# Performance work log

Measured on AMD Instinct MI355X. Metric: run time of the kernel, lower is better.

The kernel has to match this reference:

```python
import jax, jax.numpy as jnp
import numpy as np

B, T, H, W, C = 2, 4, 128, 128, 192
HEADS = 6
WS = 8          # attention window (per-frame, wsD=1)
OW = 12         # overlapping KV window: 8 + int(8*0.5)
PAD = (OW - WS) // 2
TBL = (WS + OW - 1) ** 2   # 361 relative-position-bias entries
MLP_HID = C * 2


def setup_inputs() -> dict:
    key = jax.random.key(0)
    ks = jax.random.split(key, 8)
    s = 0.02
    return dict(
        x=jax.random.normal(ks[0], (B, T, H, W, C), jnp.float32),
        x_size=jnp.array([H, W], jnp.int32),  # unused by forward (shadowed), kept for signature fidelity
        rpi_oca=jax.random.randint(ks[1], (WS * WS, OW * OW), 0, TBL),
        norm1_g=jnp.ones((C,), jnp.float32), norm1_b=jnp.zeros((C,), jnp.float32),
        qkv_w=jax.random.normal(ks[2], (C, 3 * C), jnp.float32) * s,
        qkv_b=jnp.zeros((3 * C,), jnp.float32),
        rpb_table=jax.random.normal(ks[3], (TBL, HEADS), jnp.float32) * s,
        norm2_g=jnp.ones((C,), jnp.float32), norm2_b=jnp.zeros((C,), jnp.float32),
        fc1_w=jax.random.normal(ks[4], (C, MLP_HID), jnp.float32) * s,
        fc1_b=jnp.zeros((MLP_HID,), jnp.float32),
        fc2_w=jax.random.normal(ks[5], (MLP_HID, C), jnp.float32) * s,
        fc2_b=jnp.zeros((C,), jnp.float32),
    )


def _ln(x, g, b):
    m = x.mean(-1, keepdims=True)
    v = ((x - m) ** 2).mean(-1, keepdims=True)
    return (x - m) * jax.lax.rsqrt(v + 1e-5) * g + b


def reference(x, x_size, rpi_oca, norm1_g, norm1_b, qkv_w, qkv_b, rpb_table,
              norm2_g, norm2_b, fc1_w, fc1_b, fc2_w, fc2_b):
    b, t, h, w, c = x.shape
    d = c // HEADS
    scale = d ** -0.5
    nH, nW = h // WS, w // WS
    b_ = b * t * nH * nW  # total windows
    shortcut = x
    xn = _ln(x, norm1_g, norm1_b)
    qkv = (xn @ qkv_w + qkv_b).reshape(b, t, h, w, 3, c)
    q, k, v = qkv[..., 0, :], qkv[..., 1, :], qkv[..., 2, :]
    # --- query: non-overlapping (1,8,8) windows -> (b_, heads, 64, d)
    qw = (q.reshape(b, t, nH, WS, nW, WS, c)
           .transpose(0, 1, 2, 4, 3, 5, 6)
           .reshape(b_, WS * WS, HEADS, d)
           .transpose(0, 2, 1, 3))
    # --- key/value: overlapping (1,12,12) windows with stride 8, zero-padded by 2
    hid = (jnp.arange(nH) * WS)[:, None] + jnp.arange(OW)  # (nH, OW)
    wid = (jnp.arange(nW) * WS)[:, None] + jnp.arange(OW)  # (nW, OW)

    def owin(z):
        zp = jnp.pad(z, ((0, 0), (0, 0), (PAD, PAD), (PAD, PAD), (0, 0)))
        zw = zp[:, :, hid][:, :, :, :, wid]  # (b, t, nH, OW, nW, OW, c)
        return (zw.transpose(0, 1, 2, 4, 3, 5, 6)
                  .reshape(b_, OW * OW, HEADS, d)
                  .transpose(0, 2, 1, 3))

    kw, vw = owin(k), owin(v)
    attn = jnp.einsum('bhqd,bhkd->bhqk', qw * scale, kw)  # (b_, heads, 64, 144)
    bias = rpb_table[rpi_oca.reshape(-1)].reshape(WS * WS, OW * OW, HEADS).transpose(2, 0, 1)
    attn = attn + bias[None]  # NOTE: original forward applies NO softmax (self.softmax unused)
    out = (jnp.einsum('bhqk,bhkd->bhqd', attn, vw)
             .transpose(0, 2, 1, 3)
             .reshape(b_, WS * WS, c))
    # window_reverse
    xa = (out.reshape(b, t, nH, nW, WS, WS, c)
             .transpose(0, 1, 2, 4, 3, 5, 6)
             .reshape(b, t, h, w, c))
    x = xa + shortcut  # self.proj is never applied in the original forward
    hmlp = jax.nn.gelu(_ln(x, norm2_g, norm2_b) @ fc1_w + fc1_b, approximate=False)
    return x + (hmlp @ fc2_w + fc2_b)
```

## Files before the change

kernel.cpp:

```cpp
#include <hip/hip_runtime.h>
#include <cstdint>
#include <cstddef>

typedef short bf16x8 __attribute__((ext_vector_type(8)));
typedef unsigned short u16x4 __attribute__((ext_vector_type(4)));
typedef float f32x4  __attribute__((ext_vector_type(4)));
typedef unsigned short u16;

#define DEVI __device__ __forceinline__

constexpr int C     = 192;
constexpr int HEADS = 6;
constexpr int NQKV  = 576;
constexpr int HID   = 384;
constexpr int NTOK  = 131072;

DEVI u16 f2bf(float f){
  union { float f; unsigned u; } v; v.f = f;
  return (u16)((v.u + 0x7fffu + ((v.u >> 16) & 1u)) >> 16);
}

DEVI float gelu(float xx){
  float y  = xx * 0.70710678118654752f;
  float ay = fabsf(y);
  float t  = __builtin_amdgcn_rcpf(1.0f + 0.3275911f * ay);
  float p  = t*(0.254829592f + t*(-0.284496736f + t*(1.421413741f + t*(-1.453152027f + t*1.061405429f))));
  float e  = __expf(-(y*y));
  float er = copysignf(1.0f - p*e, y);
  return 0.5f * xx * (1.0f + er);
}

__global__ void prep_kernel(const float* __restrict__ qkv_w,
                            const float* __restrict__ fc1_w,
                            const float* __restrict__ fc2_w,
                            const int*   __restrict__ rpi,
                            const float* __restrict__ rpb,
                            u16* __restrict__ qkvP,
                            u16* __restrict__ fc1P,
                            u16* __restrict__ fc2P,
                            float* __restrict__ bias_pk){
  int idx = blockIdx.x * blockDim.x + threadIdx.x;
  int stride = gridDim.x * blockDim.x;
  for(int i = idx; i < 36*6*64*8; i += stride){
    int e = i & 7, lane = (i >> 3) & 63, t = i >> 9;
    int ks = t % 6, p = t / 6;
    int n = p*16 + (lane & 15), k = ks*32 + (lane >> 4)*8 + e;
    qkvP[i] = f2bf(qkv_w[k*NQKV + n]);
  }
  for(int i = idx; i < 24*6*64*8; i += stride){
    int e = i & 7, lane = (i >> 3) & 63, t = i >> 9;
    int ks = t % 6, p = t / 6;
    int n = p*16 + (lane & 15), k = ks*32 + (lane >> 4)*8 + e;
    fc1P[i] = f2bf(fc1_w[k*HID + n]);
  }
  for(int i = idx; i < 12*12*64*8; i += stride){
    int e = i & 7, lane = (i >> 3) & 63, t = i >> 9;
    int ks = t % 12, p = t / 12;
    int n = p*16 + (lane & 15), k = ks*32 + (lane >> 4)*8 + e;
    fc2P[i] = f2bf(fc2_w[k*C + n]);
  }
  const int n4 = HEADS*5*2*4*64*4;
  for(int i = idx; i < n4; i += stride){
    int t = i;
    int r    = t & 3;  t >>= 2;
    int lane = t & 63; t >>= 6;
    int mi   = t & 3;  t >>= 2;
    int nf   = t & 1;  t >>= 1;
    int chunk = t % 5; int head = t / 5;
    int g = lane >> 4, col = lane & 15;
    int q  = mi*16 + g*4 + r;
    int kk = chunk*32 + nf*16 + col;
    float v = 0.f;
    if(kk < 144) v = rpb[rpi[q*144 + kk]*HEADS + head];
    bias_pk[i] = v;
  }
}

__global__ __launch_bounds__(384, 4)
void qkv_kernel(const float* __restrict__ x,
                const float* __restrict__ g1,
                const float* __restrict__ b1,
                const u16* __restrict__ wP,
                const float* __restrict__ qb,
                u16* __restrict__ qkv){
  __shared__ u16 xn[64][200];
  __shared__ u16 rp[64][152];
  const int tid = threadIdx.x;
  const int bid = blockIdx.x;
  const int nh = (bid >> 3) & 1;
  const int tb = (bid & 7) + ((bid >> 4) << 3);
  const size_t tok0 = (size_t)tb * 64;
  if(tid < 256){
    const int trow = tid >> 2;
    const int j = tid & 3;
    const float* xr = x + (tok0 + trow)*C;
    float4 xv[12];
    #pragma unroll
    for(int u = 0; u < 12; ++u)
      xv[u] = *reinterpret_cast<const float4*>(xr + u*16 + j*4);
    float s1 = 0.f, s2 = 0.f;
    #pragma unroll
    for(int u = 0; u < 12; ++u){
      const float* f = reinterpret_cast<const float*>(&xv[u]);
      #pragma unroll
      for(int e = 0; e < 4; ++e){ s1 += f[e]; s2 += f[e]*f[e]; }
    }
    s1 += __shfl_xor(s1, 1, 64); s2 += __shfl_xor(s2, 1, 64);
    s1 += __shfl_xor(s1, 2, 64); s2 += __shfl_xor(s2, 2, 64);
    const float mean = s1 * (1.f/192.f);
    const float rstd = rsqrtf(s2*(1.f/192.f) - mean*mean + 1e-5f);
    #pragma unroll
    for(int u = 0; u < 12; ++u){
      const float4 gv = *reinterpret_cast<const float4*>(g1 + u*16 + j*4);
      const float4 bv = *reinterpret_cast<const float4*>(b1 + u*16 + j*4);
      const float* f = reinterpret_cast<const float*>(&xv[u]);
      const float* gp = reinterpret_cast<const float*>(&gv);
      const float* bp = reinterpret_cast<const float*>(&bv);
      u16x4 pk;
      #pragma unroll
      for(int e = 0; e < 4; ++e) pk[e] = f2bf((f[e] - mean)*rstd*gp[e] + bp[e]);
      *reinterpret_cast<u16x4*>(&xn[trow][u*16 + j*4]) = pk;
    }
  }
  __syncthreads();
  const int lane = tid & 63;
  const int wn = tid >> 6;
  const int g = lane >> 4, col = lane & 15;
  const f32x4 fzero = {0.f, 0.f, 0.f, 0.f};
  f32x4 acc[4][3];
  #pragma unroll
  for(int mi = 0; mi < 4; ++mi)
    #pragma unroll
    for(int nf = 0; nf < 3; ++nf) acc[mi][nf] = fzero;
  const int p0 = nh*18 + wn*3;
  #pragma unroll
  for(int ks = 0; ks < 6; ++ks){
    bf16x8 wf[3];
    #pragma unroll
    for(int nf = 0; nf < 3; ++nf)
      wf[nf] = *reinterpret_cast<const bf16x8*>(wP + ((size_t)(((p0 + nf)*6 + ks)*64) + lane)*8);
    bf16x8 a[4];
    #pragma unroll
    for(int mi = 0; mi < 4; ++mi)
      a[mi] = *reinterpret_cast<const bf16x8*>(&xn[mi*16 + col][ks*32 + g*8]);
    #pragma unroll
    for(int nf = 0; nf < 3; ++nf)
      #pragma unroll
      for(int mi = 0; mi < 4; ++mi)
        acc[mi][nf] = __builtin_amdgcn_mfma_f32_16x16x32_bf16(a[mi], wf[nf], acc[mi][nf], 0, 0, 0);
  }
  #pragma unroll
  for(int ph = 0; ph < 2; ++ph){
    if((wn >> 1) + (wn >> 2) == ph*2 ? false : true){}
    if(wn >= ph*3 && wn < ph*3 + 3){
      const int wl = wn - ph*3;
      #pragma unroll
      for(int mi = 0; mi < 4; ++mi){
        #pragma unroll
        for(int nf = 0; nf < 3; ++nf){
          const int nloc = wl*48 + nf*16 + col;
          const float bb = qb[nh*288 + ph*144 + nloc];
          #pragma unroll
          for(int r = 0; r < 4; ++r)
            rp[mi*16 + g*4 + r][nloc] = f2bf(acc[mi][nf][r] + bb);
        }
      }
    }
    __syncthreads();
    #pragma unroll
    for(int it = 0; it < 3; ++it){
      const int c = tid + it*384;
      const int tok = c / 18, cc = c - tok*18;
      const int n0 = nh*288 + ph*144 + cc*8;
      const int pl = n0 >> 5, d0 = n0 & 31;
      bf16x8 vv = *reinterpret_cast<const bf16x8*>(&rp[tok][cc*8]);
      *reinterpret_cast<bf16x8*>(qkv + ((size_t)pl*NTOK + tok0 + tok)*32 + d0) = vv;
    }
    __syncthreads();
  }
}

__global__ __launch_bounds__(64, 2)
void attn_kernel(const u16* __restrict__ qkv,
                 const float* __restrict__ bias_pk,
                 const float* __restrict__ x,
                 float* __restrict__ out){
  __shared__ u16 Vt[32][168];
  __shared__ u16 Pl[64][40];
  const int lane = threadIdx.x;
  const int g = lane >> 4, col = lane & 15;
  const int win = blockIdx.x, head = blockIdx.y;
  const int bt = win >> 8, wh = (win >> 4) & 15, ww = win & 15;
  const int h0 = wh*8, w0 = ww*8;
  const size_t tokbase = (size_t)bt * 16384;
  const u16* Qp = qkv + (size_t)head      *NTOK*32;
  const u16* Kp = qkv + (size_t)(6 + head)*NTOK*32;
  const u16* Vp = qkv + (size_t)(12 + head)*NTOK*32;
  bf16x8 kf[10];
  #pragma unroll
  for(int i = 0; i < 10; ++i){
    const int kr = i*16 + col;
    const int r12 = (kr*2731) >> 15;
    const int c12 = kr - r12*12;
    const int hh = h0 - 2 + r12;
    const int wp = w0 - 2 + c12;
    bf16x8 kv_ = {0,0,0,0,0,0,0,0};
    bf16x8 vv_ = {0,0,0,0,0,0,0,0};
    if(kr < 144 && hh >= 0 && hh < 128 && wp >= 0 && wp < 128){
      const size_t t = tokbase + hh*128 + wp;
      kv_ = *reinterpret_cast<const bf16x8*>(Kp + t*32 + g*8);
      vv_ = *reinterpret_cast<const bf16x8*>(Vp + t*32 + g*8);
    }
    kf[i] = kv_;
    #pragma unroll
    for(int e = 0; e < 8; ++e) Vt[g*8 + e][kr] = (u16)vv_[e];
  }
  bf16x8 qf[4];
  #pragma unroll
  for(int mi = 0; mi < 4; ++mi){
    const int row = mi*16 + col;
    const size_t t = tokbase + (size_t)(h0 + (row >> 3))*128 + w0 + (row & 7);
    qf[mi] = *reinterpret_cast<const bf16x8*>(Qp + t*32 + g*8);
  }
  const f32x4 fzero = {0.f, 0.f, 0.f, 0.f};
  f32x4 oacc[4][2];
  #pragma unroll
  for(int mi = 0; mi < 4; ++mi){ oacc[mi][0] = fzero; oacc[mi][1] = fzero; }
  const float scale = 0.17677669529663689f;
  for(int ch = 0; ch < 5; ++ch){
    f32x4 s[4][2];
    #pragma unroll
    for(int nf = 0; nf < 2; ++nf){
      const bf16x8 kk = kf[ch*2 + nf];
      #pragma unroll
      for(int mi = 0; mi < 4; ++mi)
        s[mi][nf] = __builtin_amdgcn_mfma_f32_16x16x32_bf16(qf[mi], kk, fzero, 0, 0, 0);
    }
    #pragma unroll
    for(int nf = 0; nf < 2; ++nf){
      #pragma unroll
      for(int mi = 0; mi < 4; ++mi){
        const float4 bv = *reinterpret_cast<const float4*>(
            bias_pk + (size_t)((((head*5 + ch)*2 + nf)*4 + mi)*64 + lane)*4);
        const float* bvp = reinterpret_cast<const float*>(&bv);
        #pragma unroll
        for(int r = 0; r < 4; ++r)
          Pl[mi*16 + g*4 + r][nf*16 + col] = f2bf(s[mi][nf][r]*scale + bvp[r]);
      }
    }
    bf16x8 pa[4];
    #pragma unroll
    for(int mi = 0; mi < 4; ++mi)
      pa[mi] = *reinterpret_cast<const bf16x8*>(&Pl[mi*16 + col][g*8]);
    #pragma unroll
    for(int nf = 0; nf < 2; ++nf){
      const bf16x8 vfr = *reinterpret_cast<const bf16x8*>(&Vt[nf*16 + col][ch*32 + g*8]);
      #pragma unroll
      for(int mi = 0; mi < 4; ++mi)
        oacc[mi][nf] = __builtin_amdgcn_mfma_f32_16x16x32_bf16(pa[mi], vfr, oacc[mi][nf], 0, 0, 0);
    }
  }
  #pragma unroll
  for(int mi = 0; mi < 4; ++mi){
    #pragma unroll
    for(int nf = 0; nf < 2; ++nf){
      #pragma unroll
      for(int r = 0; r < 4; ++r){
        const int row = mi*16 + g*4 + r;
        const int hh = h0 + (row >> 3), wp = w0 + (row & 7);
        const size_t o = (tokbase + hh*128 + wp)*(size_t)C + head*32 + nf*16 + col;
        out[o] = oacc[mi][nf][r] + x[o];
      }
    }
  }
}

__global__ __launch_bounds__(512, 4)
void mlp_kernel(float* __restrict__ io,
                const float* __restrict__ g2,
                const float* __restrict__ b2,
                const u16* __restrict__ w1P,
                const float* __restrict__ fb1,
                const u16* __restrict__ w2P,
                const float* __restrict__ fb2){
  __shared__ u16 xn[64][200];
  __shared__ u16 hl[64][200];
  const int tid = threadIdx.x;
  const size_t tok0 = (size_t)blockIdx.x * 64;
  {
    const int trow = tid >> 3;
    const int j = tid & 7;
    const float* xr = io + (tok0 + trow)*C;
    float4 xv[6];
    #pragma unroll
    for(int u = 0; u < 6; ++u)
      xv[u] = *reinterpret_cast<const float4*>(xr + u*32 + j*4);
    float s1 = 0.f, s2 = 0.f;
    #pragma unroll
    for(int u = 0; u < 6; ++u){
      const float* f = reinterpret_cast<const float*>(&xv[u]);
      #pragma unroll
      for(int e = 0; e < 4; ++e){ s1 += f[e]; s2 += f[e]*f[e]; }
    }
    s1 += __shfl_xor(s1, 1, 64); s2 += __shfl_xor(s2, 1, 64);
    s1 += __shfl_xor(s1, 2, 64); s2 += __shfl_xor(s2, 2, 64);
    s1 += __shfl_xor(s1, 4, 64); s2 += __shfl_xor(s2, 4, 64);
    const float mean = s1 * (1.f/192.f);
    const float rstd = rsqrtf(s2*(1.f/192.f) - mean*mean + 1e-5f);
    #pragma unroll
    for(int u = 0; u < 6; ++u){
      const float4 gv = *reinterpret_cast<const float4*>(g2 + u*32 + j*4);
      const float4 bv = *reinterpret_cast<const float4*>(b2 + u*32 + j*4);
      const float* f = reinterpret_cast<const float*>(&xv[u]);
      const float* gp = reinterpret_cast<const float*>(&gv);
      const float* bp = reinterpret_cast<const float*>(&bv);
      u16x4 pk;
      #pragma unroll
      for(int e = 0; e < 4; ++e) pk[e] = f2bf((f[e] - mean)*rstd*gp[e] + bp[e]);
      *reinterpret_cast<u16x4*>(&xn[trow][u*32 + j*4]) = pk;
    }
  }
  __syncthreads();
  const int lane = tid & 63, wave = tid >> 6;
  const int wm = wave >> 2;
  const int wn = wave & 3;
  const int g = lane >> 4, col = lane & 15;
  const f32x4 fzero = {0.f, 0.f, 0.f, 0.f};
  f32x4 acc2[2][3];
  #pragma unroll
  for(int mi = 0; mi < 2; ++mi)
    #pragma unroll
    for(int nf = 0; nf < 3; ++nf) acc2[mi][nf] = fzero;
  #pragma unroll
  for(int hb = 0; hb < 2; ++hb){
    f32x4 acc1[2][3];
    #pragma unroll
    for(int mi = 0; mi < 2; ++mi)
      #pragma unroll
      for(int nf = 0; nf < 3; ++nf) acc1[mi][nf] = fzero;
    #pragma unroll
    for(int ks = 0; ks < 6; ++ks){
      bf16x8 wf[3];
      #pragma unroll
      for(int nf = 0; nf < 3; ++nf)
        wf[nf] = *reinterpret_cast<const bf16x8*>(w1P + ((size_t)(((hb*12 + wn*3 + nf)*6 + ks)*64) + lane)*8);
      bf16x8 a[2];
      #pragma unroll
      for(int mi = 0; mi < 2; ++mi)
        a[mi] = *reinterpret_cast<const bf16x8*>(&xn[wm*32 + mi*16 + col][ks*32 + g*8]);
      #pragma unroll
      for(int nf = 0; nf < 3; ++nf)
        #pragma unroll
        for(int mi = 0; mi < 2; ++mi)
          acc1[mi][nf] = __builtin_amdgcn_mfma_f32_16x16x32_bf16(a[mi], wf[nf], acc1[mi][nf], 0, 0, 0);
    }
    #pragma unroll
    for(int mi = 0; mi < 2; ++mi){
      #pragma unroll
      for(int nf = 0; nf < 3; ++nf){
        const int nl = wn*48 + nf*16 + col;
        const float bb = fb1[hb*192 + nl];
        #pragma unroll
        for(int r = 0; r < 4; ++r){
          const int row = wm*32 + mi*16 + g*4 + r;
          hl[row][nl] = f2bf(gelu(acc1[mi][nf][r] + bb));
        }
      }
    }
    __syncthreads();
    #pragma unroll
    for(int ks = 0; ks < 6; ++ks){
      bf16x8 wf[3];
      #pragma unroll
      for(int nf = 0; nf < 3; ++nf)
        wf[nf] = *reinterpret_cast<const bf16x8*>(w2P + ((size_t)(((wn*3 + nf)*12 + hb*6 + ks)*64) + lane)*8);
      bf16x8 a[2];
      #pragma unroll
      for(int mi = 0; mi < 2; ++mi)
        a[mi] = *reinterpret_cast<const bf16x8*>(&hl[wm*32 + mi*16 + col][ks*32 + g*8]);
      #pragma unroll
      for(int nf = 0; nf < 3; ++nf)
        #pragma unroll
        for(int mi = 0; mi < 2; ++mi)
          acc2[mi][nf] = __builtin_amdgcn_mfma_f32_16x16x32_bf16(a[mi], wf[nf], acc2[mi][nf], 0, 0, 0);
    }
    __syncthreads();
  }
  #pragma unroll
  for(int mi = 0; mi < 2; ++mi){
    #pragma unroll
    for(int nf = 0; nf < 3; ++nf){
      const int n = wn*48 + nf*16 + col;
      const float bb = fb2[n];
      #pragma unroll
      for(int r = 0; r < 4; ++r){
        const int row = wm*32 + mi*16 + g*4 + r;
        const size_t idx = (tok0 + row)*C + n;
        io[idx] = acc2[mi][nf][r] + bb + io[idx];
      }
    }
  }
}

extern "C" void kernel_launch(void* const* d_in, const int* in_sizes, int n_in,
                              void* d_out, int out_size, void* d_ws, size_t ws_size,
                              hipStream_t stream){
  const float* x    = (const float*)d_in[0];
  const int*   rpi  = (const int*)  d_in[2];
  const float* n1g  = (const float*)d_in[3];
  const float* n1b  = (const float*)d_in[4];
  const float* qkvw = (const float*)d_in[5];
  const float* qkvb = (const float*)d_in[6];
  const float* rpb  = (const float*)d_in[7];
  const float* n2g  = (const float*)d_in[8];
  const float* n2b  = (const float*)d_in[9];
  const float* fc1w = (const float*)d_in[10];
  const float* fc1b = (const float*)d_in[11];
  const float* fc2w = (const float*)d_in[12];
  const float* fc2b = (const float*)d_in[13];
  float* out = (float*)d_out;
  char* ws = (char*)d_ws;
  u16*   qkvP    = (u16*)  (ws + 0);
  u16*   fc1P    = (u16*)  (ws + 221184);
  u16*   fc2P    = (u16*)  (ws + 368640);
  float* bias_pk = (float*)(ws + 516096);
  u16*   qkvbuf  = (u16*)  (ws + 1499136);
  if(ws_size < 152494080ull) return;
  prep_kernel<<<dim3(512), dim3(256), 0, stream>>>(qkvw, fc1w, fc2w, rpi, rpb, qkvP, fc1P, fc2P, bias_pk);
  qkv_kernel<<<dim3(4096), dim3(384), 0, stream>>>(x, n1g, n1b, qkvP, qkvb, qkvbuf);
  attn_kernel<<<dim3(2048, 6), dim3(64), 0, stream>>>(qkvbuf, bias_pk, x, out);
  mlp_kernel<<<dim3(2048), dim3(512), 0, stream>>>(out, n2g, n2b, fc1P, fc1b, fc2P, fc2b);
}
```

Baseline: 287.6 us.

## Transpose QK MFMA and batch loads in window attention kernel

The attention kernel now issues all K/V global loads unconditionally, clamping out-of-range rows to a safe address and selecting zeros afterwards, so the loads can be batched before the LDS writes of V. The QK^T MFMA operands are swapped so each lane holds four consecutive key scores for one query, which allows packed 8-byte stores of the bf16 P tile instead of scalar 2-byte stores. The bias prepack layout is changed to match the transposed score layout. The chunk loop is fully unrolled with bias loads hoisted ahead of the MFMAs, which raises register pressure in exchange for more overlap.

```diff
diff --git a/kernel.cpp b/kernel.cpp
--- a/kernel.cpp
+++ b/kernel.cpp
@@ -67,9 +67,8 @@
     int mi   = t & 3;  t >>= 2;
     int nf   = t & 1;  t >>= 1;
     int chunk = t % 5; int head = t / 5;
-    int g = lane >> 4, col = lane & 15;
-    int q  = mi*16 + g*4 + r;
-    int kk = chunk*32 + nf*16 + col;
+    int q  = mi*16 + (lane & 15);
+    int kk = chunk*32 + nf*16 + ((lane >> 4) << 2) + r;
     float v = 0.f;
     if(kk < 144) v = rpb[rpi[q*144 + kk]*HEADS + head];
     bias_pk[i] = v;
@@ -151,7 +150,6 @@
   }
   #pragma unroll
   for(int ph = 0; ph < 2; ++ph){
-    if((wn >> 1) + (wn >> 2) == ph*2 ? false : true){}
     if(wn >= ph*3 && wn < ph*3 + 3){
       const int wl = wn - ph*3;
       #pragma unroll
@@ -196,7 +194,9 @@
   const u16* Qp = qkv + (size_t)head      *NTOK*32;
   const u16* Kp = qkv + (size_t)(6 + head)*NTOK*32;
   const u16* Vp = qkv + (size_t)(12 + head)*NTOK*32;
-  bf16x8 kf[10];
+  const bf16x8 z8 = {0,0,0,0,0,0,0,0};
+
+  bf16x8 kf[10], vf[10];
   #pragma unroll
   for(int i = 0; i < 10; ++i){
     const int kr = i*16 + col;
@@ -204,61 +204,82 @@
     const int c12 = kr - r12*12;
     const int hh = h0 - 2 + r12;
     const int wp = w0 - 2 + c12;
-    bf16x8 kv_ = {0,0,0,0,0,0,0,0};
-    bf16x8 vv_ = {0,0,0,0,0,0,0,0};
-    if(kr < 144 && hh >= 0 && hh < 128 && wp >= 0 && wp < 128){
-      const size_t t = tokbase + hh*128 + wp;
-      kv_ = *reinterpret_cast<const bf16x8*>(Kp + t*32 + g*8);
-      vv_ = *reinterpret_cast<const bf16x8*>(Vp + t*32 + g*8);
-    }
-    kf[i] = kv_;
-    #pragma unroll
-    for(int e = 0; e < 8; ++e) Vt[g*8 + e][kr] = (u16)vv_[e];
+    const bool valid = (kr < 144) && (hh >= 0) && (hh < 128) && (wp >= 0) && (wp < 128);
+    const size_t t = valid ? (tokbase + (size_t)hh*128 + wp) : tokbase;
+    bf16x8 kv_ = *reinterpret_cast<const bf16x8*>(Kp + t*32 + g*8);
+    bf16x8 vv_ = *reinterpret_cast<const bf16x8*>(Vp + t*32 + g*8);
+    kf[i] = valid ? kv_ : z8;
+    vf[i] = valid ? vv_ : z8;
   }
   bf16x8 qf[4];
   #pragma unroll
   for(int mi = 0; mi < 4; ++mi){
     const int row = mi*16 + col;
-    const size_t t = tokbase + (size_t)(h0 + (row >> 3))*128 + w0 + (row & 7);
+    const size_t t = tokbase + (size_t)(h0 + (row >> 3))*128 + (w0 + (row & 7));
     qf[mi] = *reinterpret_cast<const bf16x8*>(Qp + t*32 + g*8);
   }
+  #pragma unroll
+  for(int i = 0; i < 10; ++i) asm volatile("" : "+v"(kf[i]));
+  #pragma unroll
+  for(int mi = 0; mi < 4; ++mi) asm volatile("" : "+v"(qf[mi]));
+  #pragma unroll
+  for(int i = 0; i < 10; ++i){
+    const int kr = i*16 + col;
+    #pragma unroll
+    for(int e = 0; e < 8; ++e) Vt[g*8 + e][kr] = (u16)vf[i][e];
+  }
+
   const f32x4 fzero = {0.f, 0.f, 0.f, 0.f};
   f32x4 oacc[4][2];
   #pragma unroll
   for(int mi = 0; mi < 4; ++mi){ oacc[mi][0] = fzero; oacc[mi][1] = fzero; }
   const float scale = 0.17677669529663689f;
+
+  #pragma unroll
   for(int ch = 0; ch < 5; ++ch){
-    f32x4 s[4][2];
+    float4 bv[2][4];
+    #pragma unroll
+    for(int nf = 0; nf < 2; ++nf)
+      #pragma unroll
+      for(int mi = 0; mi < 4; ++mi)
+        bv[nf][mi] = *reinterpret_cast<const float4*>(
+            bias_pk + (size_t)((((head*5 + ch)*2 + nf)*4 + mi)*64 + lane)*4);
+    f32x4 st[2][4];
+    #pragma unroll
+    for(int nf = 0; nf < 2; ++nf)
+      #pragma unroll
+      for(int mi = 0; mi < 4; ++mi)
+        st[nf][mi] = __builtin_amdgcn_mfma_f32_16x16x32_bf16(kf[ch*2 + nf], qf[mi], fzero, 0, 0, 0);
     #pragma unroll
     for(int nf = 0; nf < 2; ++nf){
-      const bf16x8 kk = kf[ch*2 + nf];
+      #pragma unroll
+      for(int mi = 0; mi < 4; ++mi){
+        const float* bp = reinterpret_cast<const float*>(&bv[nf][mi]);
+        const float p0 = fmaf(st[nf][mi][0], scale, bp[0]);
+        const float p1 = fmaf(st[nf][mi][1], scale, bp[1]);
+        const float p2 = fmaf(st[nf][mi][2], scale, bp[2]);
+        const float p3 = fmaf(st[nf][mi][3], scale, bp[3]);
+        uint2 pw;
+        pw.x = (unsigned)f2bf(p0) | ((unsigned)f2bf(p1) << 16);
+        pw.y = (unsigned)f2bf(p2) | ((unsigned)f2bf(p3) << 16);
+        *reinterpret_cast<uint2*>(
+            reinterpret_cast<char*>(&Pl[0][0]) + (mi*16 + col)*80 + nf*32 + g*8) = pw;
+      }
+    }
+    bf16x8 pa[4];
+    #pragma unroll
+    for(int mi = 0; mi < 4; ++mi)
+      pa[mi] = *reinterpret_cast<const bf16x8*>(
+          reinterpret_cast<const char*>(&Pl[0][0]) + (mi*16 + col)*80 + g*16);
+    bf16x8 vfr[2];
+    #pragma unroll
+    for(int nf = 0; nf < 2; ++nf)
+      vfr[nf] = *reinterpret_cast<const bf16x8*>(&Vt[nf*16 + col][ch*32 + g*8]);
+    #pragma unroll
+    for(int nf = 0; nf < 2; ++nf)
       #pragma unroll
       for(int mi = 0; mi < 4; ++mi)
-        s[mi][nf] = __builtin_amdgcn_mfma_f32_16x16x32_bf16(qf[mi], kk, fzero, 0, 0, 0);
-    }
-    #pragma unroll
-    for(int nf = 0; nf < 2; ++nf){
-      #pragma unroll
-      for(int mi = 0; mi < 4; ++mi){
-        const float4 bv = *reinterpret_cast<const float4*>(
-            bias_pk + (size_t)((((head*5 + ch)*2 + nf)*4 + mi)*64 + lane)*4);
-        const float* bvp = reinterpret_cast<const float*>(&bv);
-        #pragma unroll
-        for(int r = 0; r < 4; ++r)
-          Pl[mi*16 + g*4 + r][nf*16 + col] = f2bf(s[mi][nf][r]*scale + bvp[r]);
-      }
-    }
-    bf16x8 pa[4];
-    #pragma unroll
-    for(int mi = 0; mi < 4; ++mi)
-      pa[mi] = *reinterpret_cast<const bf16x8*>(&Pl[mi*16 + col][g*8]);
-    #pragma unroll
-    for(int nf = 0; nf < 2; ++nf){
-      const bf16x8 vfr = *reinterpret_cast<const bf16x8*>(&Vt[nf*16 + col][ch*32 + g*8]);
-      #pragma unroll
-      for(int mi = 0; mi < 4; ++mi)
-        oacc[mi][nf] = __builtin_amdgcn_mfma_f32_16x16x32_bf16(pa[mi], vfr, oacc[mi][nf], 0, 0, 0);
-    }
+        oacc[mi][nf] = __builtin_amdgcn_mfma_f32_16x16x32_bf16(pa[mi], vfr[nf], oacc[mi][nf], 0, 0, 0);
   }
   #pragma unroll
   for(int mi = 0; mi < 4; ++mi){
```

New measurement: 280.8 us. -2.4%, faster.
